# Performance work log

Hardware: AMD Instinct MI355X
Metric: run time of the kernel (lower is better)

Reference implementation:

```python
import jax, jax.numpy as jnp
import numpy as np

B, CQ, CKV, H, W = 8, 256, 512, 64, 64
HKV, WKV = 32, 32
DQK = CQ // 8  # 32


def setup_inputs() -> dict:
    key = jax.random.key(0)
    ks = jax.random.split(key, 9)
    s = 0.05
    return {
        "query": jax.random.normal(ks[0], (B, CQ, H, W), jnp.float32),
        "key_value": jax.random.normal(ks[1], (B, CKV, HKV, WKV), jnp.float32),
        "Wq": jax.random.normal(ks[2], (DQK, CQ), jnp.float32) * s,
        "bq": jax.random.normal(ks[3], (DQK,), jnp.float32) * s,
        "Wk": jax.random.normal(ks[4], (DQK, CKV), jnp.float32) * s,
        "bk": jax.random.normal(ks[5], (DQK,), jnp.float32) * s,
        "Wv": jax.random.normal(ks[6], (CQ, CKV), jnp.float32) * s,
        "bv": jax.random.normal(ks[7], (CQ,), jnp.float32) * s,
        "gamma": jax.random.normal(ks[8], (1,), jnp.float32) * 0.5,
    }


def reference(query, key_value, Wq, bq, Wk, bk, Wv, bv, gamma):
    b, cq, h, w = query.shape
    n = h * w
    # bilinear resize of key_value to query's spatial size (align_corners=False
    # half-pixel convention, matching torch F.interpolate and jax.image.resize)
    kv = jax.image.resize(key_value, (b, key_value.shape[1], h, w), method="bilinear")
    # 1x1 convs are channel contractions
    q = jnp.einsum("bchw,dc->bdhw", query, Wq) + bq[None, :, None, None]   # [B,DQK,H,W]
    k = jnp.einsum("bchw,dc->bdhw", kv, Wk) + bk[None, :, None, None]      # [B,DQK,H,W]
    v = jnp.einsum("bchw,dc->bdhw", kv, Wv) + bv[None, :, None, None]      # [B,CQ,H,W]
    qf = q.reshape(b, -1, n)   # [B,DQK,N]
    kf = k.reshape(b, -1, n)   # [B,DQK,N]
    vf = v.reshape(b, -1, n)   # [B,CQ,N]
    energy = jnp.einsum("bdn,bdm->bnm", qf, kf)        # [B,N,N]
    attention = jax.nn.softmax(energy, axis=-1)
    out = jnp.einsum("bnm,bcm->bcn", attention, vf)     # [B,CQ,N]
    out = out.reshape(b, cq, h, w)
    return gamma[0] * out + query
```

## Files before the change

### kernel.cpp

```cpp
#include <hip/hip_runtime.h>

#define B_ 8
#define CQ_ 256
#define CKV_ 512
#define N_ 4096
#define DQK_ 32

typedef __bf16 bf16;
typedef __bf16 bf16x4 __attribute__((ext_vector_type(4)));
typedef __bf16 bf16x8 __attribute__((ext_vector_type(8)));
typedef float f32x4 __attribute__((ext_vector_type(4)));

__global__ void k_convert_w(const float* __restrict__ Wq, const float* __restrict__ Wk,
                            const float* __restrict__ Wv,
                            bf16* __restrict__ wq, bf16* __restrict__ wk, bf16* __restrict__ wv) {
    int i = blockIdx.x * 256 + threadIdx.x;
    if (i < 8192) wq[i] = (bf16)Wq[i];
    else if (i < 24576) wk[i - 8192] = (bf16)Wk[i - 8192];
    else if (i < 155648) wv[i - 24576] = (bf16)Wv[i - 24576];
}

__global__ __launch_bounds__(256) void k_resize(const float* __restrict__ kv, bf16* __restrict__ kvr) {
    const int yo = blockIdx.x;
    const int b  = blockIdx.y;
    const int tid = threadIdx.x;
    __shared__ float r0[64][33];
    __shared__ float r1[64][33];
    int ty = yo >> 1;
    int y0, y1; float wy0, wy1;
    if ((yo & 1) == 0) { y0 = ty > 0 ? ty - 1 : 0; y1 = ty; wy0 = 0.25f; wy1 = 0.75f; }
    else               { y0 = ty; y1 = ty < 31 ? ty + 1 : 31; wy0 = 0.75f; wy1 = 0.25f; }
    const int u_loc = tid & 63;
    const int xo_base = tid >> 6;
    for (int uc = 0; uc < CKV_; uc += 64) {
        __syncthreads();
        for (int i = 0; i < 8; ++i) {
            int idx = tid + i * 256;
            int u = idx >> 5, x = idx & 31;
            const float* src = kv + ((size_t)b * CKV_ + uc + u) * 1024 + x;
            r0[u][x] = src[y0 * 32];
            r1[u][x] = src[y1 * 32];
        }
        __syncthreads();
        for (int i = 0; i < 16; ++i) {
            int xo = xo_base + i * 4;
            int tx = xo >> 1;
            int xa, xb; float wxa, wxb;
            if ((xo & 1) == 0) { xa = tx > 0 ? tx - 1 : 0; xb = tx; wxa = 0.25f; wxb = 0.75f; }
            else               { xa = tx; xb = tx < 31 ? tx + 1 : 31; wxa = 0.75f; wxb = 0.25f; }
            float v0 = wxa * r0[u_loc][xa] + wxb * r0[u_loc][xb];
            float v1 = wxa * r1[u_loc][xa] + wxb * r1[u_loc][xb];
            float val = wy0 * v0 + wy1 * v1;
            kvr[((size_t)b * N_ + yo * 64 + xo) * CKV_ + uc + u_loc] = (bf16)val;
        }
    }
}

__global__ __launch_bounds__(256) void k_proj_q_fused(const float* __restrict__ query,
                                                      const bf16* __restrict__ W,
                                                      const float* __restrict__ bias,
                                                      bf16* __restrict__ qTb) {
    __shared__ bf16 tile[64][264];
    const int n0 = blockIdx.x * 64;
    const int b  = blockIdx.y;
    const int tid = threadIdx.x;
    const int xi = tid & 15, c0 = tid >> 4;
    for (int pass = 0; pass < 16; ++pass) {
        int c = c0 + pass * 16;
        const float4 v = *(const float4*)(query + ((size_t)b * CQ_ + c) * N_ + n0 + xi * 4);
        tile[xi * 4 + 0][c] = (bf16)v.x;
        tile[xi * 4 + 1][c] = (bf16)v.y;
        tile[xi * 4 + 2][c] = (bf16)v.z;
        tile[xi * 4 + 3][c] = (bf16)v.w;
    }
    __syncthreads();
    const int w = tid >> 6, lane = tid & 63;
    const int l16 = lane & 15, quad = lane >> 4;
    const int ct = w & 1, nh = w >> 1;
    f32x4 acc[2];
    acc[0] = (f32x4){0.f, 0.f, 0.f, 0.f}; acc[1] = (f32x4){0.f, 0.f, 0.f, 0.f};
    const bf16* aptr = W + (ct * 16 + l16) * CQ_ + quad * 8;
#pragma unroll
    for (int ks = 0; ks < 8; ++ks) {
        bf16x8 af = *(const bf16x8*)(aptr + ks * 32);
        for (int j = 0; j < 2; ++j) {
            bf16x8 bfv = *(const bf16x8*)&tile[nh * 32 + j * 16 + l16][ks * 32 + quad * 8];
            acc[j] = __builtin_amdgcn_mfma_f32_16x16x32_bf16(af, bfv, acc[j], 0, 0, 0);
        }
    }
    for (int j = 0; j < 2; ++j)
        for (int r = 0; r < 4; ++r) {
            int d = ct * 16 + quad * 4 + r;
            int n = n0 + nh * 32 + j * 16 + l16;
            qTb[((size_t)b * N_ + n) * DQK_ + d] = (bf16)(acc[j][r] + bias[d]);
        }
}

__global__ __launch_bounds__(256) void k_proj_k(const bf16* __restrict__ W,
                                                const float* __restrict__ bias,
                                                const bf16* __restrict__ Bm,
                                                bf16* __restrict__ outT) {
    const int mb = blockIdx.x * 128;
    const int b  = blockIdx.y;
    const int tid = threadIdx.x;
    const int w = tid >> 6, lane = tid & 63;
    const int l16 = lane & 15, quad = lane >> 4;
    const int ct = w & 1;
    const int mhalf = (w >> 1) * 64;
    f32x4 acc[4];
    for (int j = 0; j < 4; ++j) acc[j] = (f32x4){0.f, 0.f, 0.f, 0.f};
    const bf16* aptr  = W + (ct * 16 + l16) * CKV_ + quad * 8;
    const bf16* bbase = Bm + ((size_t)b * N_ + mb + mhalf) * CKV_ + quad * 8;
#pragma unroll
    for (int ks = 0; ks < 16; ++ks) {
        bf16x8 af = *(const bf16x8*)(aptr + ks * 32);
        for (int j = 0; j < 4; ++j) {
            bf16x8 bfv = *(const bf16x8*)(bbase + (size_t)(j * 16 + l16) * CKV_ + ks * 32);
            acc[j] = __builtin_amdgcn_mfma_f32_16x16x32_bf16(af, bfv, acc[j], 0, 0, 0);
        }
    }
    for (int j = 0; j < 4; ++j)
        for (int r = 0; r < 4; ++r) {
            int d = ct * 16 + quad * 4 + r;
            int m = mb + mhalf + j * 16 + l16;
            outT[((size_t)b * N_ + m) * DQK_ + d] = (bf16)(acc[j][r] + bias[d]);
        }
}

__global__ __launch_bounds__(256) void k_proj_v(const bf16* __restrict__ W,
                                                const float* __restrict__ bias,
                                                const bf16* __restrict__ Bm,
                                                bf16* __restrict__ vout) {
    const int mb = blockIdx.x * 64;
    const int b  = blockIdx.y;
    const int tid = threadIdx.x;
    const int w = tid >> 6, lane = tid & 63;
    const int l16 = lane & 15, quad = lane >> 4;
    f32x4 acc[4][4];
    for (int i = 0; i < 4; ++i) for (int j = 0; j < 4; ++j) acc[i][j] = (f32x4){0.f, 0.f, 0.f, 0.f};
    const bf16* bbase = Bm + ((size_t)b * N_ + mb) * CKV_ + quad * 8;
#pragma unroll 4
    for (int ks = 0; ks < 16; ++ks) {
        bf16x8 bfv[4];
        for (int j = 0; j < 4; ++j)
            bfv[j] = *(const bf16x8*)(bbase + (size_t)(j * 16 + l16) * CKV_ + ks * 32);
        for (int i = 0; i < 4; ++i) {
            bf16x8 af = *(const bf16x8*)(W + (size_t)((w * 4 + i) * 16 + l16) * CKV_ + ks * 32 + quad * 8);
            for (int j = 0; j < 4; ++j)
                acc[i][j] = __builtin_amdgcn_mfma_f32_16x16x32_bf16(af, bfv[j], acc[i][j], 0, 0, 0);
        }
    }
    for (int i = 0; i < 4; ++i)
        for (int r = 0; r < 4; ++r) {
            int c = (w * 4 + i) * 16 + quad * 4 + r;
            float bvs = bias[c];
            for (int j = 0; j < 4; ++j) {
                int m = mb + j * 16 + l16;
                vout[((size_t)b * CQ_ + c) * N_ + m] = (bf16)(acc[i][j][r] + bvs);
            }
        }
}

__global__ __launch_bounds__(256) void k_flash(const bf16* __restrict__ qT,
                                               const bf16* __restrict__ kT,
                                               const bf16* __restrict__ vv,
                                               const float* __restrict__ query,
                                               const float* __restrict__ gamma,
                                               float* __restrict__ out) {
    __shared__ bf16 P[4][64][72];
    const int b  = blockIdx.y;
    const int n0 = blockIdx.x * 64;
    const int tid = threadIdx.x;
    const int w = tid >> 6, lane = tid & 63;
    const int l16 = lane & 15, quad = lane >> 4;
    const int swz = l16 & 3;

    bf16x8 qfrag[4];
    for (int jn = 0; jn < 4; ++jn)
        qfrag[jn] = *(const bf16x8*)(qT + ((size_t)b * N_ + n0 + jn * 16 + l16) * DQK_ + quad * 8);

    f32x4 acc[4][4];
    for (int i = 0; i < 4; ++i) for (int j = 0; j < 4; ++j) acc[i][j] = (f32x4){0.f, 0.f, 0.f, 0.f};
    f32x4 lsum4[4];
    for (int j = 0; j < 4; ++j) lsum4[j] = (f32x4){0.f, 0.f, 0.f, 0.f};

    const bf16* kbase = kT + (size_t)b * N_ * DQK_;
    const bf16* vbase = vv + ((size_t)b * CQ_ + w * 64) * N_;
    bf16 (* __restrict__ Pw)[72] = P[w];

    for (int mt = 0; mt < 64; ++mt) {
        const int m0 = mt * 64;
        bf16x8 kf[4];
        for (int im = 0; im < 4; ++im)
            kf[im] = *(const bf16x8*)(kbase + (size_t)(m0 + im * 16 + l16) * DQK_ + quad * 8);
        bf16x8 vf[2][4];
        for (int ks = 0; ks < 2; ++ks)
            for (int i = 0; i < 4; ++i)
                vf[ks][i] = *(const bf16x8*)(vbase + (size_t)(i * 16 + l16) * N_ + m0 + ks * 32 + quad * 8);
        for (int jn = 0; jn < 4; ++jn) {
            for (int im = 0; im < 4; ++im) {
                f32x4 s = __builtin_amdgcn_mfma_f32_16x16x32_bf16(kf[im], qfrag[jn],
                                                                  (f32x4){0.f, 0.f, 0.f, 0.f}, 0, 0, 0);
                bf16x4 pk;
                for (int r = 0; r < 4; ++r) {
                    float p = __expf(s[r]);
                    lsum4[jn][r] += p;
                    pk[r] = (bf16)p;
                }
                *(bf16x4*)&Pw[jn * 16 + l16][((im ^ swz) << 4) + quad * 4] = pk;
            }
        }
        for (int ks = 0; ks < 2; ++ks) {
            bf16x8 pf[4];
            for (int j = 0; j < 4; ++j)
                pf[j] = *(const bf16x8*)&Pw[j * 16 + l16]
                            [((((ks << 1) | (quad >> 1)) ^ swz) << 4) + ((quad & 1) << 3)];
            for (int i = 0; i < 4; ++i)
                for (int j = 0; j < 4; ++j)
                    acc[i][j] = __builtin_amdgcn_mfma_f32_16x16x32_bf16(vf[ks][i], pf[j], acc[i][j], 0, 0, 0);
        }
    }
    float linv[4];
    for (int j = 0; j < 4; ++j) {
        float s = (lsum4[j][0] + lsum4[j][1]) + (lsum4[j][2] + lsum4[j][3]);
        s += __shfl_xor(s, 16);
        s += __shfl_xor(s, 32);
        linv[j] = 1.f / s;
    }
    const float g = gamma[0];
    for (int i = 0; i < 4; ++i)
        for (int r = 0; r < 4; ++r) {
            int c = w * 64 + i * 16 + quad * 4 + r;
            for (int j = 0; j < 4; ++j) {
                int n = n0 + j * 16 + l16;
                size_t idx = ((size_t)b * CQ_ + c) * N_ + n;
                out[idx] = g * acc[i][j][r] * linv[j] + query[idx];
            }
        }
}

extern "C" void kernel_launch(void* const* d_in, const int* in_sizes, int n_in,
                              void* d_out, int out_size, void* d_ws, size_t ws_size,
                              hipStream_t stream) {
    const float* query     = (const float*)d_in[0];
    const float* key_value = (const float*)d_in[1];
    const float* Wq = (const float*)d_in[2];
    const float* bq = (const float*)d_in[3];
    const float* Wk = (const float*)d_in[4];
    const float* bk = (const float*)d_in[5];
    const float* Wv = (const float*)d_in[6];
    const float* bv = (const float*)d_in[7];
    const float* gamma = (const float*)d_in[8];
    float* out = (float*)d_out;

    char* ws = (char*)d_ws;
    bf16* kvr  = (bf16*)(ws);
    bf16* vbuf = (bf16*)(ws + 33554432);
    bf16* qTb  = (bf16*)(ws + 50331648);
    bf16* kTb  = (bf16*)(ws + 52428800);
    bf16* wqb  = (bf16*)(ws + 54525952);
    bf16* wkb  = (bf16*)(ws + 54542336);
    bf16* wvb  = (bf16*)(ws + 54575104);

    k_convert_w<<<608, 256, 0, stream>>>(Wq, Wk, Wv, wqb, wkb, wvb);
    k_resize<<<dim3(64, 8), 256, 0, stream>>>(key_value, kvr);
    k_proj_q_fused<<<dim3(64, 8), 256, 0, stream>>>(query, wqb, bq, qTb);
    k_proj_k<<<dim3(32, 8), 256, 0, stream>>>(wkb, bk, kvr, kTb);
    k_proj_v<<<dim3(64, 8), 256, 0, stream>>>(wvb, bv, kvr, vbuf);
    k_flash<<<dim3(64, 8), 256, 0, stream>>>(qTb, kTb, vbuf, query, gamma, out);
}
```

Baseline: 345.1 us.

## Split QK^T and exp across warps with shared double-buffered P tile

Each of the four warps previously recomputed the full 64x64 score tile and its exponentials redundantly. Now each warp computes only its own 16-query slice of scores, writes it into a block-shared P tile, and all warps read the whole tile after a __syncthreads. P is double-buffered so one barrier per iteration suffices, and the next K fragment is prefetched during the loop. The change cuts redundant MFMA and exp work by a factor of four, at the cost of a block-wide barrier every iteration and cross-warp row sums exchanged through shared memory.

```diff
diff --git a/kernel.cpp b/kernel.cpp
--- a/kernel.cpp
+++ b/kernel.cpp
@@ -167,7 +167,8 @@
                                                const float* __restrict__ query,
                                                const float* __restrict__ gamma,
                                                float* __restrict__ out) {
-    __shared__ bf16 P[4][64][72];
+    __shared__ bf16 P[2][64][72];
+    __shared__ float linvs[64];
     const int b  = blockIdx.y;
     const int n0 = blockIdx.x * 64;
     const int tid = threadIdx.x;
@@ -175,58 +176,60 @@
     const int l16 = lane & 15, quad = lane >> 4;
     const int swz = l16 & 3;
 
-    bf16x8 qfrag[4];
-    for (int jn = 0; jn < 4; ++jn)
-        qfrag[jn] = *(const bf16x8*)(qT + ((size_t)b * N_ + n0 + jn * 16 + l16) * DQK_ + quad * 8);
+    const bf16x8 qfrag = *(const bf16x8*)(qT + ((size_t)b * N_ + n0 + w * 16 + l16) * DQK_ + quad * 8);
 
     f32x4 acc[4][4];
     for (int i = 0; i < 4; ++i) for (int j = 0; j < 4; ++j) acc[i][j] = (f32x4){0.f, 0.f, 0.f, 0.f};
-    f32x4 lsum4[4];
-    for (int j = 0; j < 4; ++j) lsum4[j] = (f32x4){0.f, 0.f, 0.f, 0.f};
+    f32x4 lsum = (f32x4){0.f, 0.f, 0.f, 0.f};
 
     const bf16* kbase = kT + (size_t)b * N_ * DQK_;
     const bf16* vbase = vv + ((size_t)b * CQ_ + w * 64) * N_;
-    bf16 (* __restrict__ Pw)[72] = P[w];
+
+    bf16x8 kf[4];
+    for (int im = 0; im < 4; ++im)
+        kf[im] = *(const bf16x8*)(kbase + (size_t)(im * 16 + l16) * DQK_ + quad * 8);
 
     for (int mt = 0; mt < 64; ++mt) {
         const int m0 = mt * 64;
-        bf16x8 kf[4];
-        for (int im = 0; im < 4; ++im)
-            kf[im] = *(const bf16x8*)(kbase + (size_t)(m0 + im * 16 + l16) * DQK_ + quad * 8);
+        bf16 (* __restrict__ Pb)[72] = P[mt & 1];
+        for (int im = 0; im < 4; ++im) {
+            f32x4 s = __builtin_amdgcn_mfma_f32_16x16x32_bf16(kf[im], qfrag,
+                                                              (f32x4){0.f, 0.f, 0.f, 0.f}, 0, 0, 0);
+            bf16x4 pk;
+            for (int r = 0; r < 4; ++r) {
+                float p = __expf(s[r]);
+                lsum[r] += p;
+                pk[r] = (bf16)p;
+            }
+            *(bf16x4*)&Pb[w * 16 + l16][((im ^ swz) << 4) + quad * 4] = pk;
+        }
         bf16x8 vf[2][4];
         for (int ks = 0; ks < 2; ++ks)
             for (int i = 0; i < 4; ++i)
                 vf[ks][i] = *(const bf16x8*)(vbase + (size_t)(i * 16 + l16) * N_ + m0 + ks * 32 + quad * 8);
-        for (int jn = 0; jn < 4; ++jn) {
-            for (int im = 0; im < 4; ++im) {
-                f32x4 s = __builtin_amdgcn_mfma_f32_16x16x32_bf16(kf[im], qfrag[jn],
-                                                                  (f32x4){0.f, 0.f, 0.f, 0.f}, 0, 0, 0);
-                bf16x4 pk;
-                for (int r = 0; r < 4; ++r) {
-                    float p = __expf(s[r]);
-                    lsum4[jn][r] += p;
-                    pk[r] = (bf16)p;
-                }
-                *(bf16x4*)&Pw[jn * 16 + l16][((im ^ swz) << 4) + quad * 4] = pk;
-            }
-        }
+        const int m1 = (mt + 1 < 64 ? mt + 1 : 0) * 64;
+        bf16x8 kn[4];
+        for (int im = 0; im < 4; ++im)
+            kn[im] = *(const bf16x8*)(kbase + (size_t)(m1 + im * 16 + l16) * DQK_ + quad * 8);
+        __syncthreads();
         for (int ks = 0; ks < 2; ++ks) {
             bf16x8 pf[4];
             for (int j = 0; j < 4; ++j)
-                pf[j] = *(const bf16x8*)&Pw[j * 16 + l16]
+                pf[j] = *(const bf16x8*)&Pb[j * 16 + l16]
                             [((((ks << 1) | (quad >> 1)) ^ swz) << 4) + ((quad & 1) << 3)];
             for (int i = 0; i < 4; ++i)
                 for (int j = 0; j < 4; ++j)
                     acc[i][j] = __builtin_amdgcn_mfma_f32_16x16x32_bf16(vf[ks][i], pf[j], acc[i][j], 0, 0, 0);
         }
-    }
+        for (int im = 0; im < 4; ++im) kf[im] = kn[im];
+    }
+    float s = (lsum[0] + lsum[1]) + (lsum[2] + lsum[3]);
+    s += __shfl_xor(s, 16);
+    s += __shfl_xor(s, 32);
+    if (quad == 0) linvs[w * 16 + l16] = 1.f / s;
+    __syncthreads();
     float linv[4];
-    for (int j = 0; j < 4; ++j) {
-        float s = (lsum4[j][0] + lsum4[j][1]) + (lsum4[j][2] + lsum4[j][3]);
-        s += __shfl_xor(s, 16);
-        s += __shfl_xor(s, 32);
-        linv[j] = 1.f / s;
-    }
+    for (int j = 0; j < 4; ++j) linv[j] = linvs[j * 16 + l16];
     const float g = gamma[0];
     for (int i = 0; i < 4; ++i)
         for (int r = 0; r < 4; ++r) {
```

New measurement: 341.8 us. No clear change (-0.9%).
